# Optimization experiments

Hardware: AMD Instinct MI355X
Metric: run time of the kernel (lower is better)

Reference implementation:

```python
import jax, jax.numpy as jnp
import numpy as np

EPS_STD = 1e-5   # PNA std aggregator epsilon
EPS_GN = 1e-5    # GraphNorm epsilon


def setup_inputs() -> dict:
    key = jax.random.key(0)
    B, N, C = 8, 256, 128
    ks = jax.random.split(key, 8)
    w = lambda k, sh: jax.random.normal(k, sh, jnp.float32) * 0.05
    return {
        "x": jax.random.normal(ks[0], (B, N, C), jnp.float32),
        "edge": jax.random.normal(ks[1], (B, N * N, C), jnp.float32),
        "W_edge": w(ks[2], (C, C)), "b_edge": jnp.zeros((C,), jnp.float32),
        "W_pre": w(ks[3], (3 * C, C)), "b_pre": jnp.zeros((C,), jnp.float32),
        "W_post": w(ks[4], (5 * C, C)), "b_post": jnp.zeros((C,), jnp.float32),
        "W_lin": w(ks[5], (C, C)), "b_lin": jnp.zeros((C,), jnp.float32),
        "gn_weight": jnp.ones((C,), jnp.float32),
        "gn_bias": jnp.zeros((C,), jnp.float32),
        "gn_alpha": jnp.ones((C,), jnp.float32),
    }


def reference(x, edge, W_edge, b_edge, W_pre, b_pre, W_post, b_post,
              W_lin, b_lin, gn_weight, gn_bias, gn_alpha):
    B, N, C = x.shape
    res = x
    # edge e = i*N + j: source j -> target i  => reshape to [B, i(target), j(source), C]
    e = edge.reshape(B, N, N, C)
    e_enc = e @ W_edge + b_edge                               # edge_encoder
    x_i = jnp.broadcast_to(x[:, :, None, :], (B, N, N, C))    # target feats
    x_j = jnp.broadcast_to(x[:, None, :, :], (B, N, N, C))    # source feats
    h = jnp.concatenate([x_i, x_j, e_enc], axis=-1)           # [B,N,N,3C]
    m = h @ W_pre + b_pre                                     # pre-MLP messages [B,N,N,C]
    # PNA aggregators over source axis j (graph is fully connected, degree == N)
    mean = m.mean(axis=2)
    mn = m.min(axis=2)
    mx = m.max(axis=2)
    var = (m * m).mean(axis=2) - mean * mean
    std = jnp.sqrt(jax.nn.relu(var) + EPS_STD)
    agg = jnp.concatenate([mean, mn, mx, std], axis=-1)       # [B,N,4C]
    out = jnp.concatenate([x, agg], axis=-1) @ W_post + b_post  # post-MLP [B,N,C]
    out = out @ W_lin + b_lin                                  # final linear
    # GraphNorm with batch=None in the original: stats over ALL B*N nodes
    flat = out.reshape(B * N, C)
    mu = flat.mean(axis=0, keepdims=True)
    centered = flat - gn_alpha * mu
    v = (centered * centered).mean(axis=0, keepdims=True)
    normed = gn_weight * centered / jnp.sqrt(v + EPS_GN) + gn_bias
    y = jax.nn.relu(normed).reshape(B, N, C)
    return y + res
```

## Files before the change

### kernel.cpp

```cpp
#include <hip/hip_runtime.h>
#include <hip/hip_bf16.h>
#include <stdint.h>

typedef __attribute__((ext_vector_type(8))) short bf16x8;
typedef __attribute__((ext_vector_type(4))) float f32x4;
typedef __attribute__((ext_vector_type(4))) unsigned int u32x4;

#define NB 256
#define CC 128

static __device__ __forceinline__ unsigned int cvt_pk_bf16(float lo, float hi) {
  unsigned int r;
  asm("v_cvt_pk_bf16_f32 %0, %1, %2" : "=v"(r) : "v"(lo), "v"(hi));
  return r;
}
static __device__ __forceinline__ uint16_t f2bf(float f) {
  unsigned u = __builtin_bit_cast(unsigned, f);
  return (uint16_t)((u + 0x7FFFu + ((u >> 16) & 1u)) >> 16);
}

__global__ void k_prep(const float* __restrict__ W_edge, const float* __restrict__ b_edge,
                       const float* __restrict__ W_pre, const float* __restrict__ b_pre,
                       const float* __restrict__ x,
                       uint16_t* __restrict__ wct, float* __restrict__ bc2,
                       float* __restrict__ At, unsigned* __restrict__ bvl) {
  const int c = threadIdx.x;
  if (blockIdx.x < 128) {
    const int k = blockIdx.x;
    float acc = 0.f;
    for (int q = 0; q < CC; ++q)
      acc += W_edge[k * CC + q] * W_pre[(2 * CC + q) * CC + c];
    wct[c * CC + k] = f2bf(acc);
    if (k == 0) {
      float a2 = b_pre[c];
      for (int q = 0; q < CC; ++q) a2 += b_edge[q] * W_pre[(2 * CC + q) * CC + c];
      bc2[c] = a2;
    }
  } else {
    const int m0 = (blockIdx.x - 128) * 2;
    __shared__ float xs[2][CC];
    xs[0][c] = x[(size_t)m0 * CC + c];
    xs[1][c] = x[(size_t)(m0 + 1) * CC + c];
    __syncthreads();
    float a0 = 0.f, a1 = 0.f, v0 = 0.f, v1 = 0.f;
#pragma unroll 4
    for (int k = 0; k < CC; ++k) {
      const float w1 = W_pre[k * CC + c];
      const float w2 = W_pre[(CC + k) * CC + c];
      a0 += xs[0][k] * w1; a1 += xs[1][k] * w1;
      v0 += xs[0][k] * w2; v1 += xs[1][k] * w2;
    }
    At[(size_t)m0 * CC + c] = a0;       At[(size_t)(m0 + 1) * CC + c] = a1;
    const float p0 = __shfl_down(v0, 16);
    const float p1 = __shfl_down(v1, 16);
    if ((c & 31) < 16) {
      const int di = (c >> 5) * 16 + (c & 15);
      bvl[(size_t)m0 * 64 + di]       = ((unsigned)f2bf(p0) << 16) | f2bf(v0);
      bvl[(size_t)(m0 + 1) * 64 + di] = ((unsigned)f2bf(p1) << 16) | f2bf(v1);
    }
  }
}

__global__ __launch_bounds__(256, 3) void k_edge(
    const float* __restrict__ edge, const uint16_t* __restrict__ wct,
    const unsigned* __restrict__ bvl, const float* __restrict__ At,
    const float* __restrict__ bc2, float* __restrict__ agg) {
  __shared__ __align__(16) char ebuf[2][32 * 272];
  __shared__ __align__(16) char bvbuf[2][32 * 272];

  const int blk  = blockIdx.x;
  const int b    = blk >> 8;
  const int tid  = threadIdx.x;
  const int lane = tid & 63;
  const int wv   = tid >> 6;
  const int g    = lane >> 4;
  const int lr   = lane & 15;
  const int cb   = wv * 32;

  bf16x8 bfr[2][4];
#pragma unroll
  for (int t = 0; t < 2; ++t) {
    const uint16_t* p1 = wct + (cb + t * 16 + lr) * CC + g * 8;
#pragma unroll
    for (int ks = 0; ks < 4; ++ks)
      bfr[t][ks] = *(const bf16x8*)(p1 + ks * 32);
  }
  asm volatile("s_waitcnt vmcnt(0)" ::: "memory");

  const char* egbase  = (const char*)(edge + (size_t)blk * (NB * CC));
  const char* bvgbase = (const char*)(bvl + (size_t)b * (NB * 64));
  const int sdst = (tid >> 3) * 272 + (tid & 7) * 32;

  f32x4 eA[4], eB[4];
  u32x4 vA0, vA1, vB0, vB1;

  auto LOADA = [&](int t) {
    const char* eg = egbase + (size_t)t * 16384 + tid * 64;
#pragma unroll
    for (int k = 0; k < 4; ++k) eA[k] = *(const f32x4*)(eg + k * 16);
    const char* bg = bvgbase + (size_t)t * 8192 + tid * 32;
    vA0 = *(const u32x4*)(bg);
    vA1 = *(const u32x4*)(bg + 16);
  };
  auto LOADB = [&](int t) {
    const char* eg = egbase + (size_t)t * 16384 + tid * 64;
#pragma unroll
    for (int k = 0; k < 4; ++k) eB[k] = *(const f32x4*)(eg + k * 16);
    const char* bg = bvgbase + (size_t)t * 8192 + tid * 32;
    vB0 = *(const u32x4*)(bg);
    vB1 = *(const u32x4*)(bg + 16);
  };
  auto STORE = [&](char* eb_, char* bb_, const f32x4* E, const u32x4& v0, const u32x4& v1) {
    u32x4 w0, w1;
    w0.x = cvt_pk_bf16(E[0].x, E[0].y); w0.y = cvt_pk_bf16(E[0].z, E[0].w);
    w0.z = cvt_pk_bf16(E[1].x, E[1].y); w0.w = cvt_pk_bf16(E[1].z, E[1].w);
    w1.x = cvt_pk_bf16(E[2].x, E[2].y); w1.y = cvt_pk_bf16(E[2].z, E[2].w);
    w1.z = cvt_pk_bf16(E[3].x, E[3].y); w1.w = cvt_pk_bf16(E[3].z, E[3].w);
    *(u32x4*)(eb_ + sdst) = w0;
    *(u32x4*)(eb_ + sdst + 16) = w1;
    *(u32x4*)(bb_ + sdst) = v0;
    *(u32x4*)(bb_ + sdst + 16) = v1;
  };

  float sum0 = 0.f, sum1 = 0.f, ssq0 = 0.f, ssq1 = 0.f;
  float mn0 = 1e30f, mn1 = 1e30f, mx0 = -1e30f, mx1 = -1e30f;

  auto COMPUTE = [&](const char* eb_, const char* bb_) {
#pragma unroll
    for (int rg = 0; rg < 2; ++rg) {
      const char* eb = eb_ + (rg * 16 + lr) * 272;
      f32x4 acc0 = {0.f, 0.f, 0.f, 0.f}, acc1 = {0.f, 0.f, 0.f, 0.f};
#pragma unroll
      for (int ks = 0; ks < 4; ++ks) {
        bf16x8 af = *(const bf16x8*)(eb + g * 16 + ks * 64);
        acc0 = __builtin_amdgcn_mfma_f32_16x16x32_bf16(af, bfr[0][ks], acc0, 0, 0, 0);
        acc1 = __builtin_amdgcn_mfma_f32_16x16x32_bf16(af, bfr[1][ks], acc1, 0, 0, 0);
      }
#pragma unroll
      for (int r = 0; r < 4; ++r) {
        const int row = rg * 16 + g * 4 + r;
        const unsigned pv = *(const unsigned*)(bb_ + row * 272 + wv * 64 + lr * 4);
        const float bv0 = __builtin_bit_cast(float, pv << 16);
        const float bv1 = __builtin_bit_cast(float, pv & 0xffff0000u);
        float s0 = acc0[r] + bv0;
        float s1 = acc1[r] + bv1;
        sum0 += s0; ssq0 = fmaf(s0, s0, ssq0);
        mn0 = fminf(mn0, s0); mx0 = fmaxf(mx0, s0);
        sum1 += s1; ssq1 = fmaf(s1, s1, ssq1);
        mn1 = fminf(mn1, s1); mx1 = fmaxf(mx1, s1);
      }
    }
  };

  LOADA(0); LOADB(1);
  __builtin_amdgcn_sched_barrier(0);

#pragma unroll 1
  for (int tt = 0; tt < 8; tt += 2) {
    __builtin_amdgcn_s_barrier();
    asm volatile("s_waitcnt vmcnt(6)" ::: "memory");
    __builtin_amdgcn_sched_barrier(0);
    STORE(ebuf[0], bvbuf[0], eA, vA0, vA1);
    asm volatile("s_waitcnt lgkmcnt(0)" ::: "memory");
    __builtin_amdgcn_sched_barrier(0);
    __builtin_amdgcn_s_barrier();
    if (tt + 2 < 8) LOADA(tt + 2);
    __builtin_amdgcn_sched_barrier(0);
    COMPUTE(ebuf[0], bvbuf[0]);
    __builtin_amdgcn_s_barrier();
    if (tt < 6) { asm volatile("s_waitcnt vmcnt(6)" ::: "memory"); }
    else        { asm volatile("s_waitcnt vmcnt(0)" ::: "memory"); }
    __builtin_amdgcn_sched_barrier(0);
    STORE(ebuf[1], bvbuf[1], eB, vB0, vB1);
    asm volatile("s_waitcnt lgkmcnt(0)" ::: "memory");
    __builtin_amdgcn_sched_barrier(0);
    __builtin_amdgcn_s_barrier();
    if (tt + 3 < 8) LOADB(tt + 3);
    __builtin_amdgcn_sched_barrier(0);
    COMPUTE(ebuf[1], bvbuf[1]);
  }

#pragma unroll
  for (int m = 16; m <= 32; m <<= 1) {
    sum0 += __shfl_xor(sum0, m); ssq0 += __shfl_xor(ssq0, m);
    mn0 = fminf(mn0, __shfl_xor(mn0, m)); mx0 = fmaxf(mx0, __shfl_xor(mx0, m));
    sum1 += __shfl_xor(sum1, m); ssq1 += __shfl_xor(ssq1, m);
    mn1 = fminf(mn1, __shfl_xor(mn1, m)); mx1 = fmaxf(mx1, __shfl_xor(mx1, m));
  }
  if (g == 0) {
#pragma unroll
    for (int t = 0; t < 2; ++t) {
      const int col = cb + t * 16 + lr;
      const float s   = t ? sum1 : sum0;
      const float q   = t ? ssq1 : ssq0;
      const float mnv = t ? mn1 : mn0;
      const float mxv = t ? mx1 : mx0;
      const float tt2 = At[blk * CC + col] + bc2[col];
      const float mean = s * (1.f / NB);
      const float var = q * (1.f / NB) - mean * mean;
      const float sd = sqrtf(fmaxf(var, 0.f) + 1e-5f);
      float* ap = agg + (size_t)blk * (4 * CC) + col;
      ap[0]      = tt2 + mean;
      ap[CC]     = tt2 + mnv;
      ap[2 * CC] = tt2 + mxv;
      ap[3 * CC] = sd;
    }
  }
}

__global__ __launch_bounds__(256) void k_post(
    const float* __restrict__ x, const float* __restrict__ agg,
    const float* __restrict__ W_post, const float* __restrict__ b_post,
    const float* __restrict__ W_lin, const float* __restrict__ b_lin,
    float* __restrict__ outl, float* __restrict__ psum, float* __restrict__ psq) {
  __shared__ float hx[4][5 * CC];
  __shared__ float o1[4][CC];
  __shared__ float pl[4][CC];
  const int blk = blockIdx.x;
  const int t = threadIdx.x;
  const int row0 = blk * 4;

  for (int idx = t; idx < 4 * 5 * CC; idx += 256) {
    int r = idx / (5 * CC), col = idx - r * (5 * CC);
    hx[r][col] = (col < CC) ? x[(size_t)(row0 + r) * CC + col]
                            : agg[(size_t)(row0 + r) * (4 * CC) + (col - CC)];
  }
  __syncthreads();

  const int c = t & (CC - 1);
  const int rh = t >> 7;
  float acc[2] = {b_post[c], b_post[c]};
  for (int k = 0; k < 5 * CC; k += 4) {
    float w0 = W_post[(k + 0) * CC + c];
    float w1 = W_post[(k + 1) * CC + c];
    float w2 = W_post[(k + 2) * CC + c];
    float w3 = W_post[(k + 3) * CC + c];
#pragma unroll
    for (int i = 0; i < 2; ++i) {
      const f32x4 h4 = *(const f32x4*)&hx[2 * i + rh][k];
      acc[i] += h4.x * w0 + h4.y * w1 + h4.z * w2 + h4.w * w3;
    }
  }
#pragma unroll
  for (int i = 0; i < 2; ++i) o1[2 * i + rh][c] = acc[i];
  __syncthreads();

  float a2[2] = {b_lin[c], b_lin[c]};
  for (int k = 0; k < CC; k += 4) {
    float w0 = W_lin[(k + 0) * CC + c];
    float w1 = W_lin[(k + 1) * CC + c];
    float w2 = W_lin[(k + 2) * CC + c];
    float w3 = W_lin[(k + 3) * CC + c];
#pragma unroll
    for (int i = 0; i < 2; ++i) {
      const f32x4 h4 = *(const f32x4*)&o1[2 * i + rh][k];
      a2[i] += h4.x * w0 + h4.y * w1 + h4.z * w2 + h4.w * w3;
    }
  }
  float ps = 0.f, pq = 0.f;
#pragma unroll
  for (int i = 0; i < 2; ++i) {
    outl[(size_t)(row0 + 2 * i + rh) * CC + c] = a2[i];
    ps += a2[i]; pq += a2[i] * a2[i];
  }
  pl[rh][c] = ps; pl[2 + rh][c] = pq;
  __syncthreads();
  if (t < CC) {
    psum[blk * CC + t] = pl[0][t] + pl[1][t];
    psq[blk * CC + t]  = pl[2][t] + pl[3][t];
  }
}

__global__ __launch_bounds__(256) void k_apply(
    const float* __restrict__ psum, const float* __restrict__ psq,
    const float* __restrict__ outl, const float* __restrict__ x,
    const float* __restrict__ gw, const float* __restrict__ gb,
    const float* __restrict__ alpha, float* __restrict__ y) {
  __shared__ float red[4][CC];
  __shared__ float smu[CC], siv[CC];
  const int t = threadIdx.x;
  const int c = t & (CC - 1);
  const int h = t >> 7;
  float s = 0.f, q = 0.f;
#pragma unroll 4
  for (int i = 0; i < 256; ++i) {
    const int r = h * 256 + i;
    s += psum[r * CC + c];
    q += psq[r * CC + c];
  }
  red[h][c] = s; red[2 + h][c] = q;
  __syncthreads();
  if (t < CC) {
    const float ss = red[0][t] + red[1][t];
    const float qq = red[2][t] + red[3][t];
    const float mu = ss * (1.f / 2048.f);
    const float ex2 = qq * (1.f / 2048.f);
    const float amu = alpha[t] * mu;
    const float v = ex2 - 2.f * amu * mu + amu * amu;
    smu[t] = amu;
    siv[t] = gw[t] / sqrtf(v + 1e-5f);
  }
  __syncthreads();
  const int row0 = blockIdx.x * 8;
#pragma unroll
  for (int r = 0; r < 8; r += 2) {
    const int idx = (row0 + r + h) * CC + c;
    const float o = outl[idx];
    const float val = (o - smu[c]) * siv[c] + gb[c];
    y[idx] = fmaxf(val, 0.f) + x[idx];
  }
}

extern "C" void kernel_launch(void* const* d_in, const int* in_sizes, int n_in,
                              void* d_out, int out_size, void* d_ws, size_t ws_size,
                              hipStream_t stream) {
  const float* x      = (const float*)d_in[0];
  const float* edge   = (const float*)d_in[1];
  const float* W_edge = (const float*)d_in[2];
  const float* b_edge = (const float*)d_in[3];
  const float* W_pre  = (const float*)d_in[4];
  const float* b_pre  = (const float*)d_in[5];
  const float* W_post = (const float*)d_in[6];
  const float* b_post = (const float*)d_in[7];
  const float* W_lin  = (const float*)d_in[8];
  const float* b_lin  = (const float*)d_in[9];
  const float* gw     = (const float*)d_in[10];
  const float* gb     = (const float*)d_in[11];
  const float* alpha  = (const float*)d_in[12];
  float* y = (float*)d_out;

  float* wsf = (float*)d_ws;
  float* bc2   = wsf;
  float* At    = wsf + 128;
  float* agg   = wsf + 262272;
  float* outl  = wsf + 1310848;
  float* psum  = wsf + 1572992;
  float* psq   = wsf + 1638528;
  uint16_t* wct = (uint16_t*)(wsf + 1704064);
  unsigned* bvl = (unsigned*)(wsf + 1712256);

  k_prep<<<1152, 128, 0, stream>>>(W_edge, b_edge, W_pre, b_pre, x, wct, bc2, At, bvl);
  k_edge<<<2048, 256, 0, stream>>>(edge, wct, bvl, At, bc2, agg);
  k_post<<<512, 256, 0, stream>>>(x, agg, W_post, b_post, W_lin, b_lin, outl, psum, psq);
  k_apply<<<256, 256, 0, stream>>>(psum, psq, outl, x, gw, gb, alpha, y);
}
```

Measured before the change: 107.9 us.

## Fold post and final linear weights, run post-MLP on bf16 MFMA, remap edge blocks

Multiplies W_post by W_lin (and folds the biases) in the prep kernel, so the post stage becomes a single 640x128 GEMM. That GEMM now runs on bf16 MFMA over 16-row tiles instead of scalar fp32 FMAs over 4-row tiles, which cuts the k_post grid from 512 to 128 blocks and shrinks the partial-statistics reduction in k_apply. The edge kernel's block index is also permuted so consecutive blocks fall in different batches. The trade-offs are bf16 rounding of the activations and the combined weights, plus extra prep blocks for the weight product.

```diff
diff --git a/kernel.cpp b/kernel.cpp
--- a/kernel.cpp
+++ b/kernel.cpp
@@ -21,9 +21,13 @@
 
 __global__ void k_prep(const float* __restrict__ W_edge, const float* __restrict__ b_edge,
                        const float* __restrict__ W_pre, const float* __restrict__ b_pre,
+                       const float* __restrict__ W_post, const float* __restrict__ b_post,
+                       const float* __restrict__ W_lin, const float* __restrict__ b_lin,
                        const float* __restrict__ x,
                        uint16_t* __restrict__ wct, float* __restrict__ bc2,
-                       float* __restrict__ At, unsigned* __restrict__ bvl) {
+                       float* __restrict__ At, unsigned* __restrict__ bvl,
+                       uint16_t* __restrict__ wcombT, float* __restrict__ bcomb) {
+  __shared__ float sh[32 * 128];
   const int c = threadIdx.x;
   if (blockIdx.x < 128) {
     const int k = blockIdx.x;
@@ -36,19 +40,19 @@
       for (int q = 0; q < CC; ++q) a2 += b_edge[q] * W_pre[(2 * CC + q) * CC + c];
       bc2[c] = a2;
     }
-  } else {
+  } else if (blockIdx.x < 1152) {
     const int m0 = (blockIdx.x - 128) * 2;
-    __shared__ float xs[2][CC];
-    xs[0][c] = x[(size_t)m0 * CC + c];
-    xs[1][c] = x[(size_t)(m0 + 1) * CC + c];
+    float* xs0 = sh; float* xs1 = sh + CC;
+    xs0[c] = x[(size_t)m0 * CC + c];
+    xs1[c] = x[(size_t)(m0 + 1) * CC + c];
     __syncthreads();
     float a0 = 0.f, a1 = 0.f, v0 = 0.f, v1 = 0.f;
 #pragma unroll 4
     for (int k = 0; k < CC; ++k) {
       const float w1 = W_pre[k * CC + c];
       const float w2 = W_pre[(CC + k) * CC + c];
-      a0 += xs[0][k] * w1; a1 += xs[1][k] * w1;
-      v0 += xs[0][k] * w2; v1 += xs[1][k] * w2;
+      a0 += xs0[k] * w1; a1 += xs1[k] * w1;
+      v0 += xs0[k] * w2; v1 += xs1[k] * w2;
     }
     At[(size_t)m0 * CC + c] = a0;       At[(size_t)(m0 + 1) * CC + c] = a1;
     const float p0 = __shfl_down(v0, 16);
@@ -58,6 +62,29 @@
       bvl[(size_t)m0 * 64 + di]       = ((unsigned)f2bf(p0) << 16) | f2bf(v0);
       bvl[(size_t)(m0 + 1) * 64 + di] = ((unsigned)f2bf(p1) << 16) | f2bf(v1);
     }
+  } else {
+    const int kb = (blockIdx.x - 1152) * 5;
+    float acc[5] = {0.f, 0.f, 0.f, 0.f, 0.f};
+    float bacc = 0.f;
+    for (int qc = 0; qc < 4; ++qc) {
+      __syncthreads();
+      for (int idx = c; idx < 32 * 128; idx += 128)
+        sh[idx] = W_lin[qc * 4096 + idx];
+      __syncthreads();
+#pragma unroll 1
+      for (int q = 0; q < 32; ++q) {
+        const float wlv = sh[q * 128 + c];
+        const int qg = qc * 32 + q;
+#pragma unroll
+        for (int k = 0; k < 5; ++k)
+          acc[k] += W_post[(size_t)(kb + k) * 128 + qg] * wlv;
+        bacc += b_post[qg] * wlv;
+      }
+    }
+#pragma unroll
+    for (int k = 0; k < 5; ++k)
+      wcombT[(size_t)c * 640 + kb + k] = f2bf(acc[k]);
+    if (blockIdx.x == 1152) bcomb[c] = bacc + b_lin[c];
   }
 }
 
@@ -68,7 +95,8 @@
   __shared__ __align__(16) char ebuf[2][32 * 272];
   __shared__ __align__(16) char bvbuf[2][32 * 272];
 
-  const int blk  = blockIdx.x;
+  const int bid  = blockIdx.x;
+  const int blk  = ((bid & 7) << 8) + (bid >> 3);
   const int b    = blk >> 8;
   const int tid  = threadIdx.x;
   const int lane = tid & 63;
@@ -210,64 +238,58 @@
 
 __global__ __launch_bounds__(256) void k_post(
     const float* __restrict__ x, const float* __restrict__ agg,
-    const float* __restrict__ W_post, const float* __restrict__ b_post,
-    const float* __restrict__ W_lin, const float* __restrict__ b_lin,
+    const uint16_t* __restrict__ wcombT, const float* __restrict__ bcomb,
     float* __restrict__ outl, float* __restrict__ psum, float* __restrict__ psq) {
-  __shared__ float hx[4][5 * CC];
-  __shared__ float o1[4][CC];
-  __shared__ float pl[4][CC];
-  const int blk = blockIdx.x;
-  const int t = threadIdx.x;
-  const int row0 = blk * 4;
-
-  for (int idx = t; idx < 4 * 5 * CC; idx += 256) {
-    int r = idx / (5 * CC), col = idx - r * (5 * CC);
-    hx[r][col] = (col < CC) ? x[(size_t)(row0 + r) * CC + col]
-                            : agg[(size_t)(row0 + r) * (4 * CC) + (col - CC)];
+  __shared__ __align__(16) char hbuf[16 * 1296];
+  const int blk = blockIdx.x, tid = threadIdx.x;
+  const int lane = tid & 63, wv = tid >> 6, g = lane >> 4, lr = lane & 15;
+  const int cb = wv * 32, row0 = blk * 16;
+
+  for (int u = tid; u < 2560; u += 256) {
+    const int row = u / 160, cu = u - row * 160;
+    f32x4 v;
+    if (cu < 32) v = *(const f32x4*)(x + (size_t)(row0 + row) * 128 + cu * 4);
+    else         v = *(const f32x4*)(agg + (size_t)(row0 + row) * 512 + (cu - 32) * 4);
+    unsigned* d = (unsigned*)(hbuf + row * 1296 + cu * 8);
+    d[0] = cvt_pk_bf16(v.x, v.y);
+    d[1] = cvt_pk_bf16(v.z, v.w);
   }
   __syncthreads();
 
-  const int c = t & (CC - 1);
-  const int rh = t >> 7;
-  float acc[2] = {b_post[c], b_post[c]};
-  for (int k = 0; k < 5 * CC; k += 4) {
-    float w0 = W_post[(k + 0) * CC + c];
-    float w1 = W_post[(k + 1) * CC + c];
-    float w2 = W_post[(k + 2) * CC + c];
-    float w3 = W_post[(k + 3) * CC + c];
-#pragma unroll
-    for (int i = 0; i < 2; ++i) {
-      const f32x4 h4 = *(const f32x4*)&hx[2 * i + rh][k];
-      acc[i] += h4.x * w0 + h4.y * w1 + h4.z * w2 + h4.w * w3;
-    }
-  }
-#pragma unroll
-  for (int i = 0; i < 2; ++i) o1[2 * i + rh][c] = acc[i];
-  __syncthreads();
-
-  float a2[2] = {b_lin[c], b_lin[c]};
-  for (int k = 0; k < CC; k += 4) {
-    float w0 = W_lin[(k + 0) * CC + c];
-    float w1 = W_lin[(k + 1) * CC + c];
-    float w2 = W_lin[(k + 2) * CC + c];
-    float w3 = W_lin[(k + 3) * CC + c];
-#pragma unroll
-    for (int i = 0; i < 2; ++i) {
-      const f32x4 h4 = *(const f32x4*)&o1[2 * i + rh][k];
-      a2[i] += h4.x * w0 + h4.y * w1 + h4.z * w2 + h4.w * w3;
-    }
-  }
-  float ps = 0.f, pq = 0.f;
-#pragma unroll
-  for (int i = 0; i < 2; ++i) {
-    outl[(size_t)(row0 + 2 * i + rh) * CC + c] = a2[i];
-    ps += a2[i]; pq += a2[i] * a2[i];
-  }
-  pl[rh][c] = ps; pl[2 + rh][c] = pq;
-  __syncthreads();
-  if (t < CC) {
-    psum[blk * CC + t] = pl[0][t] + pl[1][t];
-    psq[blk * CC + t]  = pl[2][t] + pl[3][t];
+  const uint16_t* wb0 = wcombT + (size_t)(cb + lr) * 640 + g * 8;
+  const uint16_t* wb1 = wcombT + (size_t)(cb + 16 + lr) * 640 + g * 8;
+  f32x4 acc0 = {0.f, 0.f, 0.f, 0.f}, acc1 = {0.f, 0.f, 0.f, 0.f};
+#pragma unroll
+  for (int ck = 0; ck < 5; ++ck) {
+#pragma unroll
+    for (int ks = 0; ks < 4; ++ks) {
+      bf16x8 af = *(const bf16x8*)(hbuf + lr * 1296 + ck * 256 + ks * 64 + g * 16);
+      bf16x8 b0 = *(const bf16x8*)(wb0 + ck * 128 + ks * 32);
+      bf16x8 b1 = *(const bf16x8*)(wb1 + ck * 128 + ks * 32);
+      acc0 = __builtin_amdgcn_mfma_f32_16x16x32_bf16(af, b0, acc0, 0, 0, 0);
+      acc1 = __builtin_amdgcn_mfma_f32_16x16x32_bf16(af, b1, acc1, 0, 0, 0);
+    }
+  }
+  const float bc0 = bcomb[cb + lr], bc1 = bcomb[cb + 16 + lr];
+  float ps0 = 0.f, pq0 = 0.f, ps1 = 0.f, pq1 = 0.f;
+#pragma unroll
+  for (int r = 0; r < 4; ++r) {
+    const int row = g * 4 + r;
+    const float o0 = acc0[r] + bc0;
+    const float o1 = acc1[r] + bc1;
+    outl[(size_t)(row0 + row) * 128 + cb + lr] = o0;
+    outl[(size_t)(row0 + row) * 128 + cb + 16 + lr] = o1;
+    ps0 += o0; pq0 = fmaf(o0, o0, pq0);
+    ps1 += o1; pq1 = fmaf(o1, o1, pq1);
+  }
+#pragma unroll
+  for (int m = 16; m <= 32; m <<= 1) {
+    ps0 += __shfl_xor(ps0, m); pq0 += __shfl_xor(pq0, m);
+    ps1 += __shfl_xor(ps1, m); pq1 += __shfl_xor(pq1, m);
+  }
+  if (g == 0) {
+    psum[blk * 128 + cb + lr] = ps0;       psq[blk * 128 + cb + lr] = pq0;
+    psum[blk * 128 + cb + 16 + lr] = ps1;  psq[blk * 128 + cb + 16 + lr] = pq1;
   }
 }
 
@@ -283,8 +305,8 @@
   const int h = t >> 7;
   float s = 0.f, q = 0.f;
 #pragma unroll 4
-  for (int i = 0; i < 256; ++i) {
-    const int r = h * 256 + i;
+  for (int i = 0; i < 64; ++i) {
+    const int r = h * 64 + i;
     s += psum[r * CC + c];
     q += psq[r * CC + c];
   }
@@ -335,12 +357,15 @@
   float* agg   = wsf + 262272;
   float* outl  = wsf + 1310848;
   float* psum  = wsf + 1572992;
-  float* psq   = wsf + 1638528;
-  uint16_t* wct = (uint16_t*)(wsf + 1704064);
-  unsigned* bvl = (unsigned*)(wsf + 1712256);
-
-  k_prep<<<1152, 128, 0, stream>>>(W_edge, b_edge, W_pre, b_pre, x, wct, bc2, At, bvl);
+  float* psq   = wsf + 1589376;
+  uint16_t* wct = (uint16_t*)(wsf + 1605760);
+  unsigned* bvl = (unsigned*)(wsf + 1613952);
+  uint16_t* wcombT = (uint16_t*)(wsf + 1745024);
+  float* bcomb = wsf + 1785984;
+
+  k_prep<<<1280, 128, 0, stream>>>(W_edge, b_edge, W_pre, b_pre, W_post, b_post,
+                                   W_lin, b_lin, x, wct, bc2, At, bvl, wcombT, bcomb);
   k_edge<<<2048, 256, 0, stream>>>(edge, wct, bvl, At, bc2, agg);
-  k_post<<<512, 256, 0, stream>>>(x, agg, W_post, b_post, W_lin, b_lin, outl, psum, psq);
+  k_post<<<128, 256, 0, stream>>>(x, agg, wcombT, bcomb, outl, psum, psq);
   k_apply<<<256, 256, 0, stream>>>(psum, psq, outl, x, gw, gb, alpha, y);
 }
```

After: 90.35 us. 1.19x faster.
